# Kernel tuning notes

Hardware: AMD Instinct MI355X
Metric: run time of the kernel (lower is better)

## Reference

```python
import jax, jax.numpy as jnp
import numpy as np

B, N, H, NH, HD, DE = 4, 512, 512, 8, 64, 64
DFF = 4 * H
EPS = 1e-5


def setup_inputs() -> dict:
    key = jax.random.key(0)
    ks = jax.random.split(key, 32)
    w = lambda k, *s: jax.random.normal(k, s, jnp.float32) * 0.02
    inp = {}
    inp['messages'] = jax.random.normal(ks[0], (B, N, H), jnp.float32)
    inp['distance_matrix'] = jax.random.randint(ks[1], (B, N, N), 0, 201).astype(jnp.float32)
    mask = jax.random.randint(ks[2], (B, N, N), 0, 2).astype(jnp.float32)
    inp['mask'] = jnp.maximum(mask, jnp.eye(N, dtype=jnp.float32)[None])  # ensure diag visible
    inp['emb_table'] = w(ks[3], 201, DE)
    inp['Wdq'] = w(ks[4], H, DE); inp['bdq'] = jnp.zeros((H,), jnp.float32)
    inp['Wdk'] = w(ks[5], H, DE); inp['bdk'] = jnp.zeros((H,), jnp.float32)
    inp['Wq'] = w(ks[6], H, H);   inp['bq'] = jnp.zeros((H,), jnp.float32)
    inp['Wk'] = w(ks[7], H, H);   inp['bk'] = jnp.zeros((H,), jnp.float32)
    inp['Wv'] = w(ks[8], H, H);   inp['bv'] = jnp.zeros((H,), jnp.float32)
    inp['Wo'] = w(ks[9], H, H);   inp['bo'] = jnp.zeros((H,), jnp.float32)
    inp['W_ih'] = w(ks[10], 3 * H, H); inp['b_ih'] = jnp.zeros((3 * H,), jnp.float32)
    inp['W_hh'] = w(ks[11], 3 * H, H); inp['b_hh'] = jnp.zeros((3 * H,), jnp.float32)
    inp['W1'] = w(ks[12], DFF, H); inp['b1'] = jnp.zeros((DFF,), jnp.float32)
    inp['W2'] = w(ks[13], H, DFF); inp['b2'] = jnp.zeros((H,), jnp.float32)
    inp['g2'] = jnp.ones((H,), jnp.float32); inp['beta2'] = jnp.zeros((H,), jnp.float32)
    return inp


def reference(messages, distance_matrix, mask, emb_table, Wdq, bdq, Wdk, bdk,
              Wq, bq, Wk, bk, Wv, bv, Wo, bo, W_ih, b_ih, W_hh, b_hh,
              W1, b1, W2, b2, g2, beta2):
    # distance embedding lookup (B,N,N,DE)
    idx = jnp.clip(distance_matrix.astype(jnp.int32), 0, 200)
    emb = emb_table[idx]
    # mean over dim then linear == linear then mean (linear maps commute with mean)
    dq = jnp.mean(emb, axis=2) @ Wdq.T + bdq  # (B,N,H)
    dk = jnp.mean(emb, axis=1) @ Wdk.T + bdk  # (B,N,H)
    Q = ((messages + dq) @ Wq.T + bq).reshape(B, N, NH, HD).transpose(0, 2, 1, 3)
    K = ((messages + dk) @ Wk.T + bk).reshape(B, N, NH, HD).transpose(0, 2, 1, 3)
    V = (messages @ Wv.T + bv).reshape(B, N, NH, HD).transpose(0, 2, 1, 3)
    scale = 1.0 / np.sqrt(HD).astype(np.float32)
    scores = jnp.einsum('bhnd,bhmd->bhnm', Q, K) * scale
    scores = jnp.where(mask[:, None] == 0, -jnp.inf, scores)
    aw = jax.nn.softmax(scores, axis=-1)
    ao = jnp.einsum('bhnm,bhmd->bhnd', aw, V).transpose(0, 2, 1, 3).reshape(B, N, H)
    ao = ao @ Wo.T + bo
    # GRUCell: x = attn output, h = messages
    gx = ao @ W_ih.T + b_ih
    gh = messages @ W_hh.T + b_hh
    xr, xz, xn = jnp.split(gx, 3, axis=-1)
    hr, hz, hn = jnp.split(gh, 3, axis=-1)
    r = jax.nn.sigmoid(xr + hr)
    z = jax.nn.sigmoid(xz + hz)
    n = jnp.tanh(xn + r * hn)
    u = (1.0 - z) * n + z * messages
    # FFN + residual + LayerNorm
    f = jax.nn.relu(u @ W1.T + b1) @ W2.T + b2
    y = u + f
    mu = jnp.mean(y, axis=-1, keepdims=True)
    var = jnp.var(y, axis=-1, keepdims=True)
    return (y - mu) / jnp.sqrt(var + EPS) * g2 + beta2
```

## Files before the change

### kernel.cpp

```cpp
#include <hip/hip_runtime.h>
#include <hip/hip_bf16.h>
#include <math.h>

#define Bz 4
#define Nn 512
#define Hh 512
#define NHh 8
#define HDd 64
#define DEe 64
#define DFFf 2048
#define EPSs 1e-5f
#define QS 1536
#define GS 3072

typedef __attribute__((ext_vector_type(8))) short bf16x8;
typedef __attribute__((ext_vector_type(4))) short bf16x4;
typedef __attribute__((ext_vector_type(4))) float f32x4;

__device__ inline short f2bf(float x) {
    unsigned u = __builtin_bit_cast(unsigned, x);
    unsigned r = (u + 0x7FFFu + ((u >> 16) & 1u)) >> 16;
    return (short)r;
}
__device__ inline float b2f(unsigned short u) {
    unsigned v = ((unsigned)u) << 16;
    return __builtin_bit_cast(float, v);
}
__device__ inline void gld16(const void* g, void* l) {
    __builtin_amdgcn_global_load_lds(
        (const __attribute__((address_space(1))) void*)g,
        (__attribute__((address_space(3))) void*)l, 16, 0, 0);
}

struct CvtSeg { const float* src; unsigned short* dst; int n, ncols, pitch; };
struct PrepArgs {
    CvtSeg cs[10];
    const float* emb; unsigned short* embb;
    const float* dist;
    unsigned short* histq; unsigned short* histk;
    const float* Wo; unsigned short* woT;
    const float* mask; unsigned long long* mbits;
    const float* fW[3]; const float* fv[3]; const float* fb[3]; float* fo[3];
};

__global__ __launch_bounds__(256) void prep_kernel(PrepArgs a)
{
    __shared__ char lds[17408];
    int t = threadIdx.x;
    int blk = blockIdx.x;
    if (blk < 512) {
        for (int sg = 0; sg < 10; ++sg) {
            CvtSeg c = a.cs[sg];
            int n4 = c.n >> 2;
            for (int i = blk * 256 + t; i < n4; i += 512 * 256) {
                int base = i * 4;
                int row = base / c.ncols;
                int col = base - row * c.ncols;
                float4 v = *(const float4*)(c.src + base);
                ushort4 o = {(unsigned short)f2bf(v.x), (unsigned short)f2bf(v.y),
                             (unsigned short)f2bf(v.z), (unsigned short)f2bf(v.w)};
                *(ushort4*)(c.dst + (size_t)row * c.pitch + col) = o;
            }
        }
        const float sc = 1.0f / 512.0f;
        for (int i = blk * 256 + t; i < 4096; i += 512 * 256) {
            ushort4 o = {0, 0, 0, 0};
            if (i * 4 < 201 * 64) {
                float4 v = *(const float4*)(a.emb + i * 4);
                o.x = (unsigned short)f2bf(v.x * sc);
                o.y = (unsigned short)f2bf(v.y * sc);
                o.z = (unsigned short)f2bf(v.z * sc);
                o.w = (unsigned short)f2bf(v.w * sc);
            }
            *(ushort4*)(a.embb + i * 4) = o;
        }
    } else if (blk < 552) {
        int fid = blk - 512;
        int f, ob;
        if (fid < 8)       { f = 0; ob = fid * 64; }
        else if (fid < 16) { f = 1; ob = (fid - 8) * 64; }
        else               { f = 2; ob = (fid - 16) * 64; }
        int i = ob + (t >> 2), part = t & 3;
        const float* Wr = a.fW[f] + (size_t)i * 512 + part * 128;
        const float* vv = a.fv[f] + part * 128;
        float s = 0.f;
        for (int k = 0; k < 128; k += 4) {
            float4 w4 = *(const float4*)(Wr + k);
            float4 b4 = *(const float4*)(vv + k);
            s += w4.x * b4.x + w4.y * b4.y + w4.z * b4.z + w4.w * b4.w;
        }
        s += __shfl_xor(s, 1);
        s += __shfl_xor(s, 2);
        if (part == 0) a.fo[f][i] = a.fb[f][i] + s;
    } else if (blk < 616) {
        int tid = blk - 552;
        int ti = tid >> 3, tj = tid & 7;
        float (*T)[68] = (float (*)[68])lds;
        int rr = t >> 4, c4 = (t & 15) * 4;
#pragma unroll
        for (int p = 0; p < 4; ++p) {
            int r = rr + p * 16;
            float4 v = *(const float4*)(a.Wo + (size_t)(ti * 64 + r) * 512 + tj * 64 + c4);
            *(float4*)&T[r][c4] = v;
        }
        __syncthreads();
#pragma unroll
        for (int p = 0; p < 4; ++p) {
            int jr = rr + p * 16;
            ushort4 o = {(unsigned short)f2bf(T[c4 + 0][jr]),
                         (unsigned short)f2bf(T[c4 + 1][jr]),
                         (unsigned short)f2bf(T[c4 + 2][jr]),
                         (unsigned short)f2bf(T[c4 + 3][jr])};
            *(ushort4*)(a.woT + (size_t)(tj * 64 + jr) * 512 + ti * 64 + c4) = o;
        }
    } else if (blk < 2664) {
        int r = blk - 616;
        int* hist = (int*)lds;
        hist[t] = 0;
        __syncthreads();
        float2 v = *(const float2*)(a.dist + (size_t)r * 512 + t * 2);
        atomicAdd(&hist[min(max((int)v.x, 0), 200)], 1);
        atomicAdd(&hist[min(max((int)v.y, 0), 200)], 1);
        __syncthreads();
        a.histq[(size_t)r * 256 + t] = (unsigned short)f2bf((float)hist[t]);
    } else if (blk < 2792) {
        int idx = blk - 2664;
        int b = idx >> 5, jt = idx & 31;
        int j0 = jt * 16;
        int* h2 = (int*)lds;
        for (int k = t; k < 4096; k += 256) h2[k] = 0;
        __syncthreads();
        int ri = t >> 4, jj = t & 15;
        for (int i0 = 0; i0 < 512; i0 += 16) {
            float v = a.dist[(size_t)(b * 512 + i0 + ri) * 512 + j0 + jj];
            atomicAdd(&h2[jj * 256 + min(max((int)v, 0), 200)], 1);
        }
        __syncthreads();
        for (int k = t; k < 4096; k += 256) {
            int jj2 = k >> 8, bin = k & 255;
            a.histk[(size_t)(b * 512 + j0 + jj2) * 256 + bin] =
                (unsigned short)f2bf((float)h2[k]);
        }
    } else {
        int idx = blk - 2792;
        int wv = t >> 6, lane = t & 63;
#pragma unroll
        for (int i = 0; i < 16; ++i) {
            int word = (idx * 4 + wv) * 16 + i;
            int rowg = word >> 3, w = word & 7;
            float mv = a.mask[(size_t)rowg * 512 + w * 64 + lane];
            unsigned long long bits = __ballot(mv != 0.0f);
            if (lane == 0) a.mbits[word] = bits;
        }
    }
}

struct Seg {
    const unsigned short* A; const unsigned short* A2;
    const unsigned short* W;
    const float* bias; const void* res; void* C;
    int lda, lda2, ksplit, Ks, ldw, rlda, ldc, Ms;
};
struct SegArgs { Seg s[6]; };

template<int BM, int BN, int RELU, int RESM, int OUTF, int HASB>
__global__ __launch_bounds__(256) void mgf_kernel(SegArgs sa, int SW)
{
    constexpr int WM = BM / 2, WN = BN / 2;
    constexpr int MT = WM / 16, NT = WN / 16;
    constexpr int IPA = BM / 32, IPB = BN / 32;
    __shared__ unsigned short As[2][BM * 64];
    __shared__ unsigned short Bs[2][BN * 64];
    int t = threadIdx.x, lane = t & 63, wid = t >> 6;
    int wm = wid >> 1, wn = wid & 1;
    int m0 = blockIdx.y * BM, n0 = blockIdx.x * BN;
    int seg = n0 / SW;
    if (m0 >= sa.s[seg].Ms) return;
    const unsigned short* A = sa.s[seg].A;
    const unsigned short* A2 = sa.s[seg].A2;
    const unsigned short* W = sa.s[seg].W;
    int lda = sa.s[seg].lda, lda2 = sa.s[seg].lda2, ksplit = sa.s[seg].ksplit;
    int Ks = sa.s[seg].Ks, ldw = sa.s[seg].ldw;
    int nloc = n0 - seg * SW;
    int lrow8 = lane >> 3;
    int lunit = (lane & 7) ^ lrow8;

    f32x4 acc[MT][NT] = {};

    auto stage = [&](int buf, int kt) {
        const unsigned short* Asrc;
        int koff, ldaa;
        if (kt < ksplit) { Asrc = A; koff = kt; ldaa = lda; }
        else             { Asrc = A2; koff = kt - ksplit; ldaa = lda2; }
#pragma unroll
        for (int i = 0; i < IPA; ++i) {
            int c = wid * IPA + i;
            gld16(Asrc + (size_t)(m0 + c * 8 + lrow8) * ldaa + koff + lunit * 8,
                  &As[buf][c * 512]);
        }
#pragma unroll
        for (int i = 0; i < IPB; ++i) {
            int c = wid * IPB + i;
            gld16(W + (size_t)(nloc + c * 8 + lrow8) * ldw + kt + lunit * 8,
                  &Bs[buf][c * 512]);
        }
    };

    stage(0, 0);
    __syncthreads();
    int cur = 0;
    for (int kt = 0; kt < Ks; kt += 64) {
        if (kt + 64 < Ks) stage(cur ^ 1, kt + 64);
#pragma unroll
        for (int kk = 0; kk < 2; ++kk) {
            bf16x8 fa[MT], fb[NT];
            int ub = kk * 4 + (lane >> 4);
#pragma unroll
            for (int mt = 0; mt < MT; ++mt) {
                int r = wm * WM + mt * 16 + (lane & 15);
                fa[mt] = *(const bf16x8*)&As[cur][r * 64 + ((ub ^ (r & 7)) << 3)];
            }
#pragma unroll
            for (int nt = 0; nt < NT; ++nt) {
                int r = wn * WN + nt * 16 + (lane & 15);
                fb[nt] = *(const bf16x8*)&Bs[cur][r * 64 + ((ub ^ (r & 7)) << 3)];
            }
#pragma unroll
            for (int mt = 0; mt < MT; ++mt)
#pragma unroll
                for (int nt = 0; nt < NT; ++nt)
                    acc[mt][nt] = __builtin_amdgcn_mfma_f32_16x16x32_bf16(
                        fa[mt], fb[nt], acc[mt][nt], 0, 0, 0);
        }
        __syncthreads();
        cur ^= 1;
    }

    int cr = (lane >> 4) * 4, ccl = lane & 15;
    const float* bias = sa.s[seg].bias;
    const void* res = sa.s[seg].res;
    int rlda = sa.s[seg].rlda, ldc = sa.s[seg].ldc;
    void* C = sa.s[seg].C;
#pragma unroll
    for (int mt = 0; mt < MT; ++mt) {
#pragma unroll
        for (int nt = 0; nt < NT; ++nt) {
            int lcol = nloc + wn * WN + nt * 16 + ccl;
            float bv = HASB ? bias[lcol] : 0.f;
#pragma unroll
            for (int r = 0; r < 4; ++r) {
                int row = m0 + wm * WM + mt * 16 + cr + r;
                float o = acc[mt][nt][r] + bv;
                if (RESM == 1)
                    o += ((const float*)res)[(size_t)row * rlda + lcol];
                if (RESM == 2)
                    o += b2f(((const unsigned short*)res)[(size_t)row * rlda + lcol]);
                if (RELU) o = fmaxf(o, 0.f);
                if (OUTF)
                    ((float*)C)[(size_t)row * ldc + lcol] = o;
                else
                    ((unsigned short*)C)[(size_t)row * ldc + lcol] =
                        (unsigned short)f2bf(o);
            }
        }
    }
}

__global__ __launch_bounds__(256) void attn_mfma_kernel(
    const unsigned short* __restrict__ QKV,
    const unsigned long long* __restrict__ mbits,
    unsigned short* __restrict__ AO)
{
    __shared__ unsigned short Qs[64 * 64];
    __shared__ unsigned short Ks[64 * 64];
    __shared__ unsigned short Vt[64 * 64];
    __shared__ unsigned short Pl[4][16 * 72];

    int t = threadIdx.x;
    int lane = t & 63;
    int wq = t >> 6;
    int g = lane >> 4, cc = lane & 15;
    int q0 = blockIdx.x * 64;
    int h = blockIdx.y, b = blockIdx.z;

    int lr = t >> 2;
    int u0 = (t & 3) * 2;

    {
        const unsigned short* src =
            QKV + ((size_t)(b * Nn + q0 + lr)) * QS + h * HDd + u0 * 8;
        bf16x8 p0 = *(const bf16x8*)(src);
        bf16x8 p1 = *(const bf16x8*)(src + 8);
        *(bf16x8*)&Qs[lr * 64 + ((u0 ^ (lr & 7)) << 3)] = p0;
        *(bf16x8*)&Qs[lr * 64 + (((u0 + 1) ^ (lr & 7)) << 3)] = p1;
    }

    const unsigned short* Krow =
        QKV + ((size_t)(b * Nn + lr)) * QS + 512 + h * HDd + u0 * 8;
    int vkey = t >> 4;
    int vd0 = (t & 15) * 4;
    const unsigned short* Vbase =
        QKV + ((size_t)(b * Nn)) * QS + 1024 + h * HDd + vd0;
    const unsigned long long* Mb =
        mbits + ((size_t)(b * Nn + q0 + wq * 16 + cc)) * 8;

    bf16x8 kr0, kr1;
    ushort4 vr[4];
    auto issue = [&](int kc) {
        int k0 = kc * 64;
        const unsigned short* kp = Krow + (size_t)k0 * QS;
        kr0 = *(const bf16x8*)(kp);
        kr1 = *(const bf16x8*)(kp + 8);
#pragma unroll
        for (int p = 0; p < 4; ++p)
            vr[p] = *(const ushort4*)(Vbase + (size_t)(k0 + vkey + p * 16) * QS);
    };
    issue(0);
    __syncthreads();

    bf16x8 qf0 = *(bf16x8*)&Qs[(wq * 16 + cc) * 64 + (((0 * 4 + g) ^ (cc & 7)) << 3)];
    bf16x8 qf1 = *(bf16x8*)&Qs[(wq * 16 + cc) * 64 + (((1 * 4 + g) ^ (cc & 7)) << 3)];

    const float scale = 0.125f;
    float m_run = -1e30f, l_run = 0.f;
    f32x4 o[4] = {};

    for (int kc = 0; kc < 8; ++kc) {
        {
            *(bf16x8*)&Ks[lr * 64 + ((u0 ^ (lr & 7)) << 3)] = kr0;
            *(bf16x8*)&Ks[lr * 64 + (((u0 + 1) ^ (lr & 7)) << 3)] = kr1;
#pragma unroll
            for (int p = 0; p < 4; ++p) {
                int key = vkey + p * 16;
                unsigned short vals[4] = {vr[p].x, vr[p].y, vr[p].z, vr[p].w};
#pragma unroll
                for (int jj = 0; jj < 4; ++jj) {
                    int j = (jj + (t >> 2)) & 3;
                    int d = vd0 + j;
                    Vt[d * 64 + (key ^ ((d & 7) << 3))] = vals[j];
                }
            }
        }
        unsigned long long mw = Mb[kc];
        __syncthreads();
        if (kc < 7) issue(kc + 1);

        f32x4 s[4] = {};
        __builtin_amdgcn_s_setprio(1);
#pragma unroll
        for (int kt = 0; kt < 4; ++kt) {
            int rA = kt * 16 + cc;
            bf16x8 a0 = *(bf16x8*)&Ks[rA * 64 + (((0 * 4 + g) ^ (rA & 7)) << 3)];
            s[kt] = __builtin_amdgcn_mfma_f32_16x16x32_bf16(a0, qf0, s[kt], 0, 0, 0);
            bf16x8 a1 = *(bf16x8*)&Ks[rA * 64 + (((1 * 4 + g) ^ (rA & 7)) << 3)];
            s[kt] = __builtin_amdgcn_mfma_f32_16x16x32_bf16(a1, qf1, s[kt], 0, 0, 0);
        }
        __builtin_amdgcn_s_setprio(0);

        float pv[4][4];
        float tmax = -1e30f;
#pragma unroll
        for (int kt = 0; kt < 4; ++kt) {
#pragma unroll
            for (int r = 0; r < 4; ++r) {
                int kpos = kt * 16 + g * 4 + r;
                float svv = ((mw >> kpos) & 1ull) ? s[kt][r] : -1e30f;
                pv[kt][r] = svv;
                tmax = fmaxf(tmax, svv);
            }
        }
        tmax = fmaxf(tmax, __shfl_xor(tmax, 16));
        tmax = fmaxf(tmax, __shfl_xor(tmax, 32));
        float mnew = fmaxf(m_run, tmax);
        float rescale = __expf((m_run - mnew) * scale);
        float psum = 0.f;
#pragma unroll
        for (int kt = 0; kt < 4; ++kt) {
#pragma unroll
            for (int r = 0; r < 4; ++r) {
                float sv = pv[kt][r];
                float p = (sv == -1e30f) ? 0.f : __expf((sv - mnew) * scale);
                pv[kt][r] = p;
                psum += p;
            }
        }
        psum += __shfl_xor(psum, 16);
        psum += __shfl_xor(psum, 32);
        l_run = l_run * rescale + psum;
        m_run = mnew;
#pragma unroll
        for (int dt = 0; dt < 4; ++dt) {
            o[dt][0] *= rescale; o[dt][1] *= rescale;
            o[dt][2] *= rescale; o[dt][3] *= rescale;
        }

#pragma unroll
        for (int kt = 0; kt < 4; ++kt) {
            bf16x4 pk = {f2bf(pv[kt][0]), f2bf(pv[kt][1]),
                         f2bf(pv[kt][2]), f2bf(pv[kt][3])};
            *(bf16x4*)&Pl[wq][cc * 72 + kt * 16 + g * 4] = pk;
        }
        bf16x8 pf0 = *(bf16x8*)&Pl[wq][cc * 72 + 0 + g * 8];
        bf16x8 pf1 = *(bf16x8*)&Pl[wq][cc * 72 + 32 + g * 8];

        __builtin_amdgcn_s_setprio(1);
#pragma unroll
        for (int dt = 0; dt < 4; ++dt) {
            int rV = dt * 16 + cc;
            bf16x8 vf0 = *(bf16x8*)&Vt[rV * 64 + (((0 * 4 + g) ^ (rV & 7)) << 3)];
            o[dt] = __builtin_amdgcn_mfma_f32_16x16x32_bf16(vf0, pf0, o[dt], 0, 0, 0);
            bf16x8 vf1 = *(bf16x8*)&Vt[rV * 64 + (((1 * 4 + g) ^ (rV & 7)) << 3)];
            o[dt] = __builtin_amdgcn_mfma_f32_16x16x32_bf16(vf1, pf1, o[dt], 0, 0, 0);
        }
        __builtin_amdgcn_s_setprio(0);
        __syncthreads();
    }

    float invl = 1.f / l_run;
#pragma unroll
    for (int dt = 0; dt < 4; ++dt) {
        ushort4 w = {(unsigned short)f2bf(o[dt][0] * invl),
                     (unsigned short)f2bf(o[dt][1] * invl),
                     (unsigned short)f2bf(o[dt][2] * invl),
                     (unsigned short)f2bf(o[dt][3] * invl)};
        *(ushort4*)&AO[((size_t)(b * Nn + q0 + wq * 16 + cc)) * Hh +
                       h * HDd + dt * 16 + g * 4] = w;
    }
}

__global__ __launch_bounds__(256) void gru_kernel(
    const unsigned short* __restrict__ G,
    const float* __restrict__ msg, unsigned short* __restrict__ u)
{
    int i4 = blockIdx.x * 256 + threadIdx.x;
    int e = i4 * 4;
    int row = e >> 9, col = e & 511;
    const unsigned short* gxr = G + (size_t)row * GS;
    const unsigned short* ghr = gxr + 1536;
    ushort4 xr4 = *(const ushort4*)(gxr + col);
    ushort4 xz4 = *(const ushort4*)(gxr + col + 512);
    ushort4 xn4 = *(const ushort4*)(gxr + col + 1024);
    ushort4 hr4 = *(const ushort4*)(ghr + col);
    ushort4 hz4 = *(const ushort4*)(ghr + col + 512);
    ushort4 hn4 = *(const ushort4*)(ghr + col + 1024);
    float4 mg4 = *(const float4*)(msg + e);
    float mv[4] = {mg4.x, mg4.y, mg4.z, mg4.w};
    unsigned short xr[4] = {xr4.x, xr4.y, xr4.z, xr4.w};
    unsigned short xz[4] = {xz4.x, xz4.y, xz4.z, xz4.w};
    unsigned short xn[4] = {xn4.x, xn4.y, xn4.z, xn4.w};
    unsigned short hr[4] = {hr4.x, hr4.y, hr4.z, hr4.w};
    unsigned short hz[4] = {hz4.x, hz4.y, hz4.z, hz4.w};
    unsigned short hn[4] = {hn4.x, hn4.y, hn4.z, hn4.w};
    ushort4 out;
    unsigned short* op = (unsigned short*)&out;
#pragma unroll
    for (int j = 0; j < 4; ++j) {
        float r = 1.f / (1.f + __expf(-(b2f(xr[j]) + b2f(hr[j]))));
        float z = 1.f / (1.f + __expf(-(b2f(xz[j]) + b2f(hz[j]))));
        float n = tanhf(b2f(xn[j]) + r * b2f(hn[j]));
        op[j] = (unsigned short)f2bf((1.f - z) * n + z * mv[j]);
    }
    *(ushort4*)(u + e) = out;
}

__global__ __launch_bounds__(256) void ln_kernel(
    const float* __restrict__ Y, const float* __restrict__ g,
    const float* __restrict__ be, float* __restrict__ out)
{
    int row = blockIdx.x, t = threadIdx.x;
    const float* yr = Y + (size_t)row * Hh;
    float v0 = yr[t], v1 = yr[t + 256];
    float s = v0 + v1, s2 = v0 * v0 + v1 * v1;
#pragma unroll
    for (int o = 1; o < 64; o <<= 1) {
        s += __shfl_xor(s, o);
        s2 += __shfl_xor(s2, o);
    }
    __shared__ float rs[4], rs2[4];
    int w = t >> 6;
    if ((t & 63) == 0) { rs[w] = s; rs2[w] = s2; }
    __syncthreads();
    float ts = rs[0] + rs[1] + rs[2] + rs[3];
    float ts2 = rs2[0] + rs2[1] + rs2[2] + rs2[3];
    float mu = ts * (1.0f / Hh);
    float var = ts2 * (1.0f / Hh) - mu * mu;
    float rstd = rsqrtf(var + EPSs);
    out[(size_t)row * Hh + t] = (v0 - mu) * rstd * g[t] + be[t];
    out[(size_t)row * Hh + t + 256] = (v1 - mu) * rstd * g[t + 256] + be[t + 256];
}

extern "C" void kernel_launch(void* const* d_in, const int* in_sizes, int n_in,
                              void* d_out, int out_size, void* d_ws, size_t ws_size,
                              hipStream_t stream) {
    const float* messages = (const float*)d_in[0];
    const float* dist     = (const float*)d_in[1];
    const float* mask     = (const float*)d_in[2];
    const float* emb      = (const float*)d_in[3];
    const float* Wdq = (const float*)d_in[4];  const float* bdq = (const float*)d_in[5];
    const float* Wdk = (const float*)d_in[6];  const float* bdk = (const float*)d_in[7];
    const float* Wq  = (const float*)d_in[8];  const float* bq  = (const float*)d_in[9];
    const float* Wk  = (const float*)d_in[10]; const float* bk  = (const float*)d_in[11];
    const float* Wv  = (const float*)d_in[12]; const float* bv  = (const float*)d_in[13];
    const float* Wo  = (const float*)d_in[14]; const float* bo  = (const float*)d_in[15];
    const float* W_ih = (const float*)d_in[16]; const float* b_ih = (const float*)d_in[17];
    const float* W_hh = (const float*)d_in[18]; const float* b_hh = (const float*)d_in[19];
    const float* W1  = (const float*)d_in[20]; const float* b1  = (const float*)d_in[21];
    const float* W2  = (const float*)d_in[22]; const float* b2  = (const float*)d_in[23];
    const float* g2  = (const float*)d_in[24]; const float* beta2 = (const float*)d_in[25];

    const int M = Bz * Nn;
    char* ws = (char*)d_ws;

    unsigned short* wdqb  = (unsigned short*)(ws + 0);
    unsigned short* wdkb  = (unsigned short*)(ws + 65536);
    unsigned short* Wbigq = (unsigned short*)(ws + 131072);
    unsigned short* Wbigk = (unsigned short*)(ws + 917504);
    unsigned short* wvb   = (unsigned short*)(ws + 1703936);
    unsigned short* wihb  = (unsigned short*)(ws + 2228224);
    unsigned short* whhb  = (unsigned short*)(ws + 3801088);
    unsigned short* w1b   = (unsigned short*)(ws + 5373952);
    unsigned short* w2b   = (unsigned short*)(ws + 7471104);
    unsigned short* msgs  = (unsigned short*)(ws + 9568256);
    unsigned short* histq = (unsigned short*)(ws + 11665408);
    unsigned short* histk = (unsigned short*)(ws + 12713984);
    unsigned short* embb  = (unsigned short*)(ws + 13762560);
    unsigned short* EcatTq= (unsigned short*)(ws + 13795328);
    unsigned short* EcatTk= (unsigned short*)(ws + 14057472);
    unsigned short* woT   = (unsigned short*)(ws + 14319616);
    unsigned short* Wfih  = (unsigned short*)(ws + 14843904);
    unsigned short* QKVb  = (unsigned short*)(ws + 16416768);
    unsigned short* AO    = (unsigned short*)(ws + 22708224);
    unsigned short* G     = (unsigned short*)(ws + 24805376);
    unsigned short* ub    = (unsigned short*)(ws + 37388288);
    unsigned short* f1    = (unsigned short*)(ws + 39485440);
    float*          yb    = (float*)(ws + 47874048);
    float*          bqp   = (float*)(ws + 52068352);
    float*          bkp   = (float*)(ws + 52070400);
    float*          bgxp  = (float*)(ws + 52072448);
    unsigned long long* mbits = (unsigned long long*)(ws + 52078592);

    dim3 blk(256);

    PrepArgs pa;
    pa.cs[0] = {messages, msgs,  M * Hh,      512,  512};
    pa.cs[1] = {Wdq,      wdqb,  Hh * DEe,    64,   64};
    pa.cs[2] = {Wdk,      wdkb,  Hh * DEe,    64,   64};
    pa.cs[3] = {Wq,       Wbigq, Hh * Hh,     512,  768};
    pa.cs[4] = {Wk,       Wbigk, Hh * Hh,     512,  768};
    pa.cs[5] = {Wv,       wvb,   Hh * Hh,     512,  512};
    pa.cs[6] = {W_ih,     wihb,  3 * Hh * Hh, 512,  512};
    pa.cs[7] = {W_hh,     whhb,  3 * Hh * Hh, 512,  512};
    pa.cs[8] = {W1,       w1b,   DFFf * Hh,   512,  512};
    pa.cs[9] = {W2,       w2b,   Hh * DFFf,   2048, 2048};
    pa.emb = emb; pa.embb = embb;
    pa.dist = dist; pa.histq = histq; pa.histk = histk;
    pa.Wo = Wo; pa.woT = woT;
    pa.mask = mask; pa.mbits = mbits;
    pa.fW[0] = Wq;   pa.fv[0] = bdq; pa.fb[0] = bq;   pa.fo[0] = bqp;
    pa.fW[1] = Wk;   pa.fv[1] = bdk; pa.fb[1] = bk;   pa.fo[1] = bkp;
    pa.fW[2] = W_ih; pa.fv[2] = bo;  pa.fb[2] = b_ih; pa.fo[2] = bgxp;
    prep_kernel<<<3048, blk, 0, stream>>>(pa);

    {
        SegArgs sa = {};
        sa.s[0] = {embb, nullptr, wdqb, nullptr, nullptr, EcatTq,
                   64, 0, 9999, 64, 64, 0, 512, 256};
        sa.s[1] = {embb, nullptr, wdkb, nullptr, nullptr, EcatTk,
                   64, 0, 9999, 64, 64, 0, 512, 256};
        sa.s[2] = {wihb, nullptr, woT, nullptr, nullptr, Wfih,
                   512, 0, 9999, 512, 512, 0, 512, 1536};
        mgf_kernel<64, 64, 0, 0, 0, 0><<<dim3(24, 24), blk, 0, stream>>>(sa, 512);
    }

    {
        SegArgs sa = {};
        sa.s[0] = {Wbigq, nullptr, EcatTq, nullptr, nullptr, Wbigq + 512,
                   768, 0, 9999, 512, 512, 0, 768, 512};
        sa.s[1] = {Wbigk, nullptr, EcatTk, nullptr, nullptr, Wbigk + 512,
                   768, 0, 9999, 512, 512, 0, 768, 512};
        mgf_kernel<64, 64, 0, 0, 0, 0><<<dim3(8, 8), blk, 0, stream>>>(sa, 256);
    }

    {
        SegArgs sa = {};
        sa.s[0] = {msgs, histq, Wbigq,             bqp,         nullptr, QKVb,
                   512, 256, 512, 768, 768, 0, QS, 2048};
        sa.s[1] = {msgs, histk, Wbigk,             bkp,         nullptr, QKVb + 512,
                   512, 256, 512, 768, 768, 0, QS, 2048};
        sa.s[2] = {msgs, nullptr, wvb,             bv,          nullptr, QKVb + 1024,
                   512, 0, 9999, 512, 512, 0, QS, 2048};
        sa.s[3] = {msgs, nullptr, whhb,            b_hh,        nullptr, G + 1536,
                   512, 0, 9999, 512, 512, 0, GS, 2048};
        sa.s[4] = {msgs, nullptr, whhb + 512 * 512, b_hh + 512, nullptr, G + 2048,
                   512, 0, 9999, 512, 512, 0, GS, 2048};
        sa.s[5] = {msgs, nullptr, whhb + 1024 * 512, b_hh + 1024, nullptr, G + 2560,
                   512, 0, 9999, 512, 512, 0, GS, 2048};
        mgf_kernel<64, 128, 0, 0, 0, 1><<<dim3(24, 32), blk, 0, stream>>>(sa, 512);
    }

    attn_mfma_kernel<<<dim3(Nn / 64, NHh, Bz), blk, 0, stream>>>(QKVb, mbits, AO);

    {
        SegArgs sa = {};
        sa.s[0] = {AO, nullptr, Wfih, bgxp, nullptr, G,
                   512, 0, 9999, 512, 512, 0, GS, 2048};
        mgf_kernel<64, 128, 0, 0, 0, 1><<<dim3(12, 32), blk, 0, stream>>>(sa, 1536);
    }

    gru_kernel<<<(M * Hh) / 1024, blk, 0, stream>>>(G, messages, ub);

    {
        SegArgs sa = {};
        sa.s[0] = {ub, nullptr, w1b, b1, nullptr, f1,
                   512, 0, 9999, 512, 512, 0, DFFf, 2048};
        mgf_kernel<64, 128, 1, 0, 0, 1><<<dim3(16, 32), blk, 0, stream>>>(sa, 2048);
    }
    {
        SegArgs sa = {};
        sa.s[0] = {f1, nullptr, w2b, b2, ub, yb,
                   2048, 0, 9999, 2048, 2048, 512, 512, 2048};
        mgf_kernel<64, 64, 0, 2, 1, 1><<<dim3(8, 32), blk, 0, stream>>>(sa, 512);
    }

    ln_kernel<<<M, blk, 0, stream>>>(yb, g2, beta2, (float*)d_out);
}
```

Measured before the change: 120.8 us.

## Write V transposed from projection GEMM and enlarge GEMM tiles to 128x128

The V projection segment now writes its output directly in a per-head transposed layout (b,h,d,n) through a new vmode epilogue. The attention kernel can then load V rows with vectorized 16-byte loads and store them into LDS without the scalar scatter-transpose. Q and K move to a separate 1024-wide buffer. Separately, the QKV/GRU-hidden GEMM and the FFN1 GEMM switch to 128x128 tiles with half the row blocks. This raises per-block reuse but lowers the number of blocks and may raise register pressure.

```diff
diff --git a/kernel.cpp b/kernel.cpp
--- a/kernel.cpp
+++ b/kernel.cpp
@@ -10,7 +10,6 @@
 #define DEe 64
 #define DFFf 2048
 #define EPSs 1e-5f
-#define QS 1536
 #define GS 3072
 
 typedef __attribute__((ext_vector_type(8))) short bf16x8;
@@ -159,7 +158,7 @@
     const unsigned short* A; const unsigned short* A2;
     const unsigned short* W;
     const float* bias; const void* res; void* C;
-    int lda, lda2, ksplit, Ks, ldw, rlda, ldc, Ms;
+    int lda, lda2, ksplit, Ks, ldw, rlda, ldc, Ms, vmode;
 };
 struct SegArgs { Seg s[6]; };
 
@@ -240,6 +239,7 @@
     const float* bias = sa.s[seg].bias;
     const void* res = sa.s[seg].res;
     int rlda = sa.s[seg].rlda, ldc = sa.s[seg].ldc;
+    int vmode = sa.s[seg].vmode;
     void* C = sa.s[seg].C;
 #pragma unroll
     for (int mt = 0; mt < MT; ++mt) {
@@ -247,6 +247,15 @@
         for (int nt = 0; nt < NT; ++nt) {
             int lcol = nloc + wn * WN + nt * 16 + ccl;
             float bv = HASB ? bias[lcol] : 0.f;
+            if (vmode) {
+                int h = lcol >> 6, d = lcol & 63;
+                int row0 = m0 + wm * WM + mt * 16 + cr;
+                int b = row0 >> 9, n = row0 & 511;
+                bf16x4 pk = {f2bf(acc[mt][nt][0] + bv), f2bf(acc[mt][nt][1] + bv),
+                             f2bf(acc[mt][nt][2] + bv), f2bf(acc[mt][nt][3] + bv)};
+                *(bf16x4*)&((unsigned short*)C)[(((size_t)b * 8 + h) * 64 + d) * 512 + n] = pk;
+                continue;
+            }
 #pragma unroll
             for (int r = 0; r < 4; ++r) {
                 int row = m0 + wm * WM + mt * 16 + cr + r;
@@ -267,7 +276,8 @@
 }
 
 __global__ __launch_bounds__(256) void attn_mfma_kernel(
-    const unsigned short* __restrict__ QKV,
+    const unsigned short* __restrict__ QKb,
+    const unsigned short* __restrict__ VT,
     const unsigned long long* __restrict__ mbits,
     unsigned short* __restrict__ AO)
 {
@@ -288,7 +298,7 @@
 
     {
         const unsigned short* src =
-            QKV + ((size_t)(b * Nn + q0 + lr)) * QS + h * HDd + u0 * 8;
+            QKb + ((size_t)(b * Nn + q0 + lr)) * 1024 + h * HDd + u0 * 8;
         bf16x8 p0 = *(const bf16x8*)(src);
         bf16x8 p1 = *(const bf16x8*)(src + 8);
         *(bf16x8*)&Qs[lr * 64 + ((u0 ^ (lr & 7)) << 3)] = p0;
@@ -296,24 +306,20 @@
     }
 
     const unsigned short* Krow =
-        QKV + ((size_t)(b * Nn + lr)) * QS + 512 + h * HDd + u0 * 8;
-    int vkey = t >> 4;
-    int vd0 = (t & 15) * 4;
-    const unsigned short* Vbase =
-        QKV + ((size_t)(b * Nn)) * QS + 1024 + h * HDd + vd0;
+        QKb + ((size_t)(b * Nn + lr)) * 1024 + 512 + h * HDd + u0 * 8;
+    const unsigned short* Vrow =
+        VT + (((size_t)(b * 8 + h)) * 64 + lr) * 512 + u0 * 8;
     const unsigned long long* Mb =
         mbits + ((size_t)(b * Nn + q0 + wq * 16 + cc)) * 8;
 
-    bf16x8 kr0, kr1;
-    ushort4 vr[4];
+    bf16x8 kr0, kr1, vr0, vr1;
     auto issue = [&](int kc) {
         int k0 = kc * 64;
-        const unsigned short* kp = Krow + (size_t)k0 * QS;
+        const unsigned short* kp = Krow + (size_t)k0 * 1024;
         kr0 = *(const bf16x8*)(kp);
         kr1 = *(const bf16x8*)(kp + 8);
-#pragma unroll
-        for (int p = 0; p < 4; ++p)
-            vr[p] = *(const ushort4*)(Vbase + (size_t)(k0 + vkey + p * 16) * QS);
+        vr0 = *(const bf16x8*)(Vrow + k0);
+        vr1 = *(const bf16x8*)(Vrow + k0 + 8);
     };
     issue(0);
     __syncthreads();
@@ -329,17 +335,8 @@
         {
             *(bf16x8*)&Ks[lr * 64 + ((u0 ^ (lr & 7)) << 3)] = kr0;
             *(bf16x8*)&Ks[lr * 64 + (((u0 + 1) ^ (lr & 7)) << 3)] = kr1;
-#pragma unroll
-            for (int p = 0; p < 4; ++p) {
-                int key = vkey + p * 16;
-                unsigned short vals[4] = {vr[p].x, vr[p].y, vr[p].z, vr[p].w};
-#pragma unroll
-                for (int jj = 0; jj < 4; ++jj) {
-                    int j = (jj + (t >> 2)) & 3;
-                    int d = vd0 + j;
-                    Vt[d * 64 + (key ^ ((d & 7) << 3))] = vals[j];
-                }
-            }
+            *(bf16x8*)&Vt[lr * 64 + ((u0 ^ (lr & 7)) << 3)] = vr0;
+            *(bf16x8*)&Vt[lr * 64 + (((u0 + 1) ^ (lr & 7)) << 3)] = vr1;
         }
         unsigned long long mw = Mb[kc];
         __syncthreads();
@@ -528,7 +525,8 @@
     unsigned short* EcatTk= (unsigned short*)(ws + 14057472);
     unsigned short* woT   = (unsigned short*)(ws + 14319616);
     unsigned short* Wfih  = (unsigned short*)(ws + 14843904);
-    unsigned short* QKVb  = (unsigned short*)(ws + 16416768);
+    unsigned short* QKb   = (unsigned short*)(ws + 16416768);
+    unsigned short* VT    = (unsigned short*)(ws + 20611072);
     unsigned short* AO    = (unsigned short*)(ws + 22708224);
     unsigned short* G     = (unsigned short*)(ws + 24805376);
     unsigned short* ub    = (unsigned short*)(ws + 37388288);
@@ -564,46 +562,47 @@
     {
         SegArgs sa = {};
         sa.s[0] = {embb, nullptr, wdqb, nullptr, nullptr, EcatTq,
-                   64, 0, 9999, 64, 64, 0, 512, 256};
+                   64, 0, 9999, 64, 64, 0, 512, 256, 0};
         sa.s[1] = {embb, nullptr, wdkb, nullptr, nullptr, EcatTk,
-                   64, 0, 9999, 64, 64, 0, 512, 256};
+                   64, 0, 9999, 64, 64, 0, 512, 256, 0};
         sa.s[2] = {wihb, nullptr, woT, nullptr, nullptr, Wfih,
-                   512, 0, 9999, 512, 512, 0, 512, 1536};
+                   512, 0, 9999, 512, 512, 0, 512, 1536, 0};
         mgf_kernel<64, 64, 0, 0, 0, 0><<<dim3(24, 24), blk, 0, stream>>>(sa, 512);
     }
 
     {
         SegArgs sa = {};
         sa.s[0] = {Wbigq, nullptr, EcatTq, nullptr, nullptr, Wbigq + 512,
-                   768, 0, 9999, 512, 512, 0, 768, 512};
+                   768, 0, 9999, 512, 512, 0, 768, 512, 0};
         sa.s[1] = {Wbigk, nullptr, EcatTk, nullptr, nullptr, Wbigk + 512,
-                   768, 0, 9999, 512, 512, 0, 768, 512};
+                   768, 0, 9999, 512, 512, 0, 768, 512, 0};
         mgf_kernel<64, 64, 0, 0, 0, 0><<<dim3(8, 8), blk, 0, stream>>>(sa, 256);
     }
 
     {
         SegArgs sa = {};
-        sa.s[0] = {msgs, histq, Wbigq,             bqp,         nullptr, QKVb,
-                   512, 256, 512, 768, 768, 0, QS, 2048};
-        sa.s[1] = {msgs, histk, Wbigk,             bkp,         nullptr, QKVb + 512,
-                   512, 256, 512, 768, 768, 0, QS, 2048};
-        sa.s[2] = {msgs, nullptr, wvb,             bv,          nullptr, QKVb + 1024,
-                   512, 0, 9999, 512, 512, 0, QS, 2048};
+        sa.s[0] = {msgs, histq, Wbigq,             bqp,         nullptr, QKb,
+                   512, 256, 512, 768, 768, 0, 1024, 2048, 0};
+        sa.s[1] = {msgs, histk, Wbigk,             bkp,         nullptr, QKb + 512,
+                   512, 256, 512, 768, 768, 0, 1024, 2048, 0};
+        sa.s[2] = {msgs, nullptr, wvb,             bv,          nullptr, VT,
+                   512, 0, 9999, 512, 512, 0, 0, 2048, 1};
         sa.s[3] = {msgs, nullptr, whhb,            b_hh,        nullptr, G + 1536,
-                   512, 0, 9999, 512, 512, 0, GS, 2048};
+                   512, 0, 9999, 512, 512, 0, GS, 2048, 0};
         sa.s[4] = {msgs, nullptr, whhb + 512 * 512, b_hh + 512, nullptr, G + 2048,
-                   512, 0, 9999, 512, 512, 0, GS, 2048};
+                   512, 0, 9999, 512, 512, 0, GS, 2048, 0};
         sa.s[5] = {msgs, nullptr, whhb + 1024 * 512, b_hh + 1024, nullptr, G + 2560,
-                   512, 0, 9999, 512, 512, 0, GS, 2048};
-        mgf_kernel<64, 128, 0, 0, 0, 1><<<dim3(24, 32), blk, 0, stream>>>(sa, 512);
-    }
-
-    attn_mfma_kernel<<<dim3(Nn / 64, NHh, Bz), blk, 0, stream>>>(QKVb, mbits, AO);
+                   512, 0, 9999, 512, 512, 0, GS, 2048, 0};
+        mgf_kernel<128, 128, 0, 0, 0, 1><<<dim3(24, 16), blk, 0, stream>>>(sa, 512);
+    }
+
+    attn_mfma_kernel<<<dim3(Nn / 64, NHh, Bz), blk, 0, stream>>>(
+        QKb, VT, mbits, AO);
 
     {
         SegArgs sa = {};
         sa.s[0] = {AO, nullptr, Wfih, bgxp, nullptr, G,
-                   512, 0, 9999, 512, 512, 0, GS, 2048};
+                   512, 0, 9999, 512, 512, 0, GS, 2048, 0};
         mgf_kernel<64, 128, 0, 0, 0, 1><<<dim3(12, 32), blk, 0, stream>>>(sa, 1536);
     }
 
@@ -612,13 +611,13 @@
     {
         SegArgs sa = {};
         sa.s[0] = {ub, nullptr, w1b, b1, nullptr, f1,
-                   512, 0, 9999, 512, 512, 0, DFFf, 2048};
-        mgf_kernel<64, 128, 1, 0, 0, 1><<<dim3(16, 32), blk, 0, stream>>>(sa, 2048);
+                   512, 0, 9999, 512, 512, 0, DFFf, 2048, 0};
+        mgf_kernel<128, 128, 1, 0, 0, 1><<<dim3(16, 16), blk, 0, stream>>>(sa, 2048);
     }
     {
         SegArgs sa = {};
         sa.s[0] = {f1, nullptr, w2b, b2, ub, yb,
-                   2048, 0, 9999, 2048, 2048, 512, 512, 2048};
+                   2048, 0, 9999, 2048, 2048, 512, 512, 2048, 0};
         mgf_kernel<64, 64, 0, 2, 1, 1><<<dim3(8, 32), blk, 0, stream>>>(sa, 512);
     }
 
```

Measured after the change: 130.9 us. 1.08x slower.
